# Kernel optimization log

Hardware: AMD Instinct MI355X
Metric: run time of the kernel (lower is better)

## Reference

```python
import jax, jax.numpy as jnp
import numpy as np

B, T = 64, 512
OBS, DM, DS, NL = 115, 128, 8, 3
EMB, NA, H1 = 16, 19, 256


def _ln(x, g, b, eps=1e-5):
    m = jnp.mean(x, -1, keepdims=True)
    v = jnp.mean((x - m) ** 2, -1, keepdims=True)
    return (x - m) * jax.lax.rsqrt(v + eps) * g + b


def _s6(x, h, lng, lnb, w_ig, w_dt, b_dt, a_log, w_b, w_c, d_par, w_out):
    # x: [B,T,DM], h: [B,DM,DS]
    xn = _ln(x, lng, lnb)
    xp = xn @ w_ig.T                               # [B,T,2*DM]
    x_in, z = xp[..., :DM], xp[..., DM:]
    dt = jax.nn.softplus(x_in @ w_dt.T + b_dt)     # [B,T,DM]
    A = -jnp.exp(a_log)                            # [DM,DS]
    bt = x_in @ w_b.T                              # [B,T,DS]
    ct = x_in @ w_c.T                              # [B,T,DS]
    dA = jnp.exp(dt[..., None] * A)                # [B,T,DM,DS]
    upd = (dt * x_in)[..., None] * bt[:, :, None, :]  # [B,T,DM,DS]

    def step(hc, inp):
        dA_t, u_t, c_t = inp
        hn = dA_t * hc + u_t                       # [B,DM,DS]
        y = jnp.einsum('bds,bs->bd', hn, c_t)      # [B,DM]
        return hn, y

    h_f, ys = jax.lax.scan(
        step, h,
        (jnp.swapaxes(dA, 0, 1), jnp.swapaxes(upd, 0, 1), jnp.swapaxes(ct, 0, 1)))
    y = jnp.swapaxes(ys, 0, 1)                     # [B,T,DM]
    ssm = y * jax.nn.silu(z) + x_in * d_par
    return x + ssm @ w_out.T, h_f.reshape(h_f.shape[0], -1)


def _forward(prev_actions, obs, h0, enc_w1, enc_b1, enc_g1, enc_bb1, enc_w2, enc_b2,
             enc_g2, enc_bb2, emb, proj_w, proj_b, proj_g, proj_bb,
             m_ln_g, m_ln_b, m_w_ig, m_w_dt, m_b_dt, m_a_log, m_w_b, m_w_c, m_d, m_w_out,
             fn_g, fn_b, pol_w1, pol_b1, pol_g, pol_bb, pol_w2, pol_b2):
    # MLP encoder: Linear -> LN -> SiLU -> Linear -> LN (final norm)
    e = jax.nn.silu(_ln(obs @ enc_w1.T + enc_b1, enc_g1, enc_bb1))
    e = _ln(e @ enc_w2.T + enc_b2, enc_g2, enc_bb2)
    pa = emb[prev_actions]                         # [B,T,EMB]
    x = jnp.concatenate([e, pa], -1) @ proj_w.T + proj_b
    x = jax.nn.silu(_ln(x, proj_g, proj_bb))
    for i in range(NL):
        x, _ = _s6(x, h0[i].reshape(-1, DM, DS), m_ln_g[i], m_ln_b[i], m_w_ig[i],
                   m_w_dt[i], m_b_dt[i], m_a_log[i], m_w_b[i], m_w_c[i], m_d[i], m_w_out[i])
    x = _ln(x, fn_g, fn_b)
    p = jax.nn.silu(_ln(x @ pol_w1.T + pol_b1, pol_g, pol_bb))
    return p @ pol_w2.T + pol_b2                   # [B,T,NA] policy logits


def setup_inputs() -> dict:
    key = jax.random.key(0)
    ks = iter(jax.random.split(key, 64))
    def n(shape, s=0.05):
        return jax.random.normal(next(ks), shape, dtype=jnp.float32) * s
    return {
        'obs': jax.random.normal(next(ks), (B, T, OBS), dtype=jnp.float32),
        'h0': jnp.zeros((NL, B, DM * DS), jnp.float32),
        'enc_w1': n((H1, OBS)), 'enc_b1': jnp.zeros((H1,)),
        'enc_g1': jnp.ones((H1,)), 'enc_bb1': jnp.zeros((H1,)),
        'enc_w2': n((DM, H1)), 'enc_b2': jnp.zeros((DM,)),
        'enc_g2': jnp.ones((DM,)), 'enc_bb2': jnp.zeros((DM,)),
        'emb': n((NA + 1, EMB), 1.0),
        'proj_w': n((DM, DM + EMB)), 'proj_b': jnp.zeros((DM,)),
        'proj_g': jnp.ones((DM,)), 'proj_bb': jnp.zeros((DM,)),
        'm_ln_g': jnp.ones((NL, DM)), 'm_ln_b': jnp.zeros((NL, DM)),
        'm_w_ig': n((NL, 2 * DM, DM)), 'm_w_dt': n((NL, DM, DM)),
        'm_b_dt': jnp.zeros((NL, DM)),
        'm_a_log': jax.random.uniform(next(ks), (NL, DM, DS), minval=-3.0, maxval=-1.0, dtype=jnp.float32),
        'm_w_b': n((NL, DS, DM)), 'm_w_c': n((NL, DS, DM)),
        'm_d': jnp.ones((NL, DM)), 'm_w_out': n((NL, DM, DM)),
        'fn_g': jnp.ones((DM,)), 'fn_b': jnp.zeros((DM,)),
        'pol_w1': n((DM, DM)), 'pol_b1': jnp.zeros((DM,)),
        'pol_g': jnp.ones((DM,)), 'pol_bb': jnp.zeros((DM,)),
        'pol_w2': n((NA, DM)), 'pol_b2': jnp.zeros((NA,)),
        'prev_actions': jax.random.randint(next(ks), (B, T), 0, NA + 1),
    }


def reference(obs, h0, enc_w1, enc_b1, enc_g1, enc_bb1, enc_w2, enc_b2, enc_g2, enc_bb2,
              emb, proj_w, proj_b, proj_g, proj_bb, m_ln_g, m_ln_b, m_w_ig, m_w_dt,
              m_b_dt, m_a_log, m_w_b, m_w_c, m_d, m_w_out, fn_g, fn_b, pol_w1, pol_b1,
              pol_g, pol_bb, pol_w2, pol_b2, prev_actions):
    return _forward(prev_actions, obs, h0, enc_w1, enc_b1, enc_g1, enc_bb1, enc_w2,
                    enc_b2, enc_g2, enc_bb2, emb, proj_w, proj_b, proj_g, proj_bb,
                    m_ln_g, m_ln_b, m_w_ig, m_w_dt, m_b_dt, m_a_log, m_w_b, m_w_c,
                    m_d, m_w_out, fn_g, fn_b, pol_w1, pol_b1, pol_g, pol_bb, pol_w2, pol_b2)
```

## Files before the change

kernel.cpp:

```cpp
#include <hip/hip_runtime.h>
#include <math.h>

#define BB 64
#define TT 512
#define OBSD 115
#define DMD 128
#define DSD 8
#define NLD 3
#define EMBD 16
#define NAD 19
#define H1D 256
#define NTOK (BB*TT)
#define SSEG 16
#define TSEG (TT/SSEG)

typedef unsigned short ushort_t;
typedef __attribute__((ext_vector_type(8))) short short8;
typedef __attribute__((ext_vector_type(4))) float f32x4;

__device__ __forceinline__ float silu_f(float x){ return x / (1.f + __expf(-x)); }
__device__ __forceinline__ float softplus_f(float x){
  return fmaxf(x, 0.f) + log1pf(__expf(-fabsf(x)));
}
__device__ __forceinline__ ushort_t f2bf(float x){
  unsigned u = __float_as_uint(x);
  unsigned r = (u + 0x7fffu + ((u >> 16) & 1u)) >> 16;
  return (ushort_t)r;
}
__device__ __forceinline__ float b2f(ushort_t x){
  return __uint_as_float(((unsigned)x) << 16);
}
#define MFMA(a,b,c) __builtin_amdgcn_mfma_f32_16x16x32_bf16((a),(b),(c),0,0,0)
#define LOG2E 1.44269504f

template<int D, int SV>
__device__ __forceinline__ void ln32(const float* s_val, float* s_mr, int tid){
  const int t = tid >> 3, part = tid & 7;
  float s = 0.f, s2 = 0.f;
  #pragma unroll
  for (int j = part; j < D; j += 8){ float v = s_val[t*SV + j]; s += v; s2 = fmaf(v, v, s2); }
  s += __shfl_xor(s, 1, 64); s2 += __shfl_xor(s2, 1, 64);
  s += __shfl_xor(s, 2, 64); s2 += __shfl_xor(s2, 2, 64);
  s += __shfl_xor(s, 4, 64); s2 += __shfl_xor(s2, 4, 64);
  if (part == 0){
    float m = s * (1.f/(float)D);
    s_mr[t*2] = m;
    s_mr[t*2+1] = rsqrtf(s2 * (1.f/(float)D) - m*m + 1e-5f);
  }
}

struct PJob { const float* src; ushort_t* dst; int N; int K; int Kpad; int rowofs; int Nw; };
struct PJobs { PJob j[20]; };

__global__ __launch_bounds__(256) void k_prep(PJobs P){
  const int job = blockIdx.x >> 2;
  const int sub = blockIdx.x & 3;
  PJob pj = P.j[job];
  const int elems = pj.Nw * pj.Kpad;
  for (int idx = sub*256 + threadIdx.x; idx < elems; idx += 4*256){
    int n = idx / pj.Kpad;
    int k = idx - n*pj.Kpad;
    float v = (n < pj.N && k < pj.K) ? pj.src[(size_t)n*pj.K + k] : 0.f;
    pj.dst[(size_t)(pj.rowofs + n)*pj.Kpad + k] = f2bf(v);
  }
}

__global__ __launch_bounds__(256) void k_enc1(
    const float* __restrict__ obs, const ushort_t* __restrict__ w1b,
    const float* __restrict__ b1, const float* __restrict__ g1,
    const float* __restrict__ bb1, ushort_t* __restrict__ e1)
{
  __shared__ __align__(16) char sm[34048];
  float*    s_val = (float*)sm;
  ushort_t* s_a   = (ushort_t*)sm;
  float*    s_mr  = (float*)(sm + 33792);
  const int tok0 = blockIdx.x * 32;
  const int tid = threadIdx.x;
  const int lane = tid & 63, w = tid >> 6;
  const int q = lane >> 4, cn = lane & 15;
  const int m0 = (w & 1) * 16, nh = w >> 1;

  for (int e = tid; e < 32*16; e += 256){
    int t = e >> 4, kc = e & 15;
    const float* op = obs + (size_t)(tok0 + t)*OBSD;
    short8 v;
    #pragma unroll
    for (int j = 0; j < 8; j++){
      int k = kc*8 + j;
      v[j] = (short)f2bf(k < OBSD ? op[k] : 0.f);
    }
    *(short8*)&s_a[t*136 + kc*8] = v;
  }
  __syncthreads();

  short8 af[4];
  #pragma unroll
  for (int ks = 0; ks < 4; ks++)
    af[ks] = *(const short8*)&s_a[(m0 + cn)*136 + ks*32 + q*8];
  __syncthreads();

  #pragma unroll
  for (int nt = 0; nt < 8; nt++){
    const int n0 = (nh*8 + nt) * 16;
    f32x4 acc = {0.f,0.f,0.f,0.f};
    #pragma unroll
    for (int ks = 0; ks < 4; ks++){
      short8 bf = *(const short8*)&w1b[(size_t)(n0 + cn)*128 + ks*32 + q*8];
      acc = MFMA(af[ks], bf, acc);
    }
    float bias = b1[n0 + cn];
    #pragma unroll
    for (int r = 0; r < 4; r++)
      s_val[(m0 + q*4 + r)*264 + n0 + cn] = acc[r] + bias;
  }
  __syncthreads();

  ln32<256,264>(s_val, s_mr, tid);
  __syncthreads();
  for (int e = tid; e < 32*256; e += 256){
    int t = e >> 8, c = e & 255;
    float v = (s_val[t*264 + c] - s_mr[t*2]) * s_mr[t*2+1] * g1[c] + bb1[c];
    e1[(size_t)(tok0 + t)*256 + c] = f2bf(silu_f(v));
  }
}

__global__ __launch_bounds__(256) void k_enc2p(
    const ushort_t* __restrict__ e1, const ushort_t* __restrict__ w2b,
    const float* __restrict__ b2, const float* __restrict__ g2,
    const float* __restrict__ bb2,
    const float* __restrict__ emb, const int* __restrict__ pact,
    const ushort_t* __restrict__ pwb, const float* __restrict__ pb,
    const float* __restrict__ pg, const float* __restrict__ pbb,
    float* __restrict__ X,
    const float* __restrict__ lng, const float* __restrict__ lnb,
    const ushort_t* __restrict__ wigb, const ushort_t* __restrict__ wdbcb,
    const float* __restrict__ bdt,
    ushort_t* __restrict__ XINb, ushort_t* __restrict__ Zb,
    ushort_t* __restrict__ DTb, ushort_t* __restrict__ BTu, ushort_t* __restrict__ CTu,
    const float* __restrict__ alog0,
    float* __restrict__ HLOC, float* __restrict__ PPR)
{
  __shared__ __align__(16) char sm[28928];
  float*    s_val = (float*)sm;
  ushort_t* s_xin = (ushort_t*)sm;
  ushort_t* s_dt  = (ushort_t*)(sm + 8704);
  ushort_t* s_a   = (ushort_t*)(sm + 17408);
  ushort_t* s_btc = (ushort_t*)(sm + 28160);
  float*    s_mr  = (float*)(sm + 28672);

  const int tok0 = blockIdx.x * 32;
  const int bidx = blockIdx.x >> 4;
  const int ch   = blockIdx.x & 15;
  const int tid = threadIdx.x;
  const int lane = tid & 63, w = tid >> 6;
  const int q = lane >> 4, cn = lane & 15;
  const int m0 = (w & 1) * 16, nh = w >> 1;

  for (int e = tid; e < 32*32; e += 256){
    int t = e >> 5, k = e & 31;
    float v = 0.f;
    if (k < EMBD){ int a = pact[tok0 + t]; v = emb[(size_t)a*EMBD + k]; }
    s_a[t*168 + 128 + k] = f2bf(v);
  }
  {
    short8 af[8];
    #pragma unroll
    for (int ks = 0; ks < 8; ks++)
      af[ks] = *(const short8*)&e1[(size_t)(tok0 + m0 + cn)*256 + ks*32 + q*8];
    #pragma unroll
    for (int nt = 0; nt < 4; nt++){
      const int n0 = (nh*4 + nt) * 16;
      f32x4 acc = {0.f,0.f,0.f,0.f};
      #pragma unroll
      for (int ks = 0; ks < 8; ks++){
        short8 bf = *(const short8*)&w2b[(size_t)(n0 + cn)*256 + ks*32 + q*8];
        acc = MFMA(af[ks], bf, acc);
      }
      float bias = b2[n0 + cn];
      #pragma unroll
      for (int r = 0; r < 4; r++)
        s_val[(m0 + q*4 + r)*136 + n0 + cn] = acc[r] + bias;
    }
  }
  __syncthreads();

  ln32<128,136>(s_val, s_mr, tid);
  __syncthreads();
  for (int e = tid; e < 32*128; e += 256){
    int t = e >> 7, c = e & 127;
    float v = (s_val[t*136 + c] - s_mr[t*2]) * s_mr[t*2+1] * g2[c] + bb2[c];
    s_a[t*168 + c] = f2bf(v);
  }
  __syncthreads();

  {
    short8 af2[5];
    #pragma unroll
    for (int ks = 0; ks < 5; ks++)
      af2[ks] = *(const short8*)&s_a[(m0 + cn)*168 + ks*32 + q*8];
    #pragma unroll
    for (int nt = 0; nt < 4; nt++){
      const int n0 = (nh*4 + nt) * 16;
      f32x4 acc = {0.f,0.f,0.f,0.f};
      #pragma unroll
      for (int ks = 0; ks < 5; ks++){
        short8 bf = *(const short8*)&pwb[(size_t)(n0 + cn)*160 + ks*32 + q*8];
        acc = MFMA(af2[ks], bf, acc);
      }
      float bias = pb[n0 + cn];
      #pragma unroll
      for (int r = 0; r < 4; r++)
        s_val[(m0 + q*4 + r)*136 + n0 + cn] = acc[r] + bias;
    }
  }
  __syncthreads();

  ln32<128,136>(s_val, s_mr, tid);
  __syncthreads();
  for (int e = tid; e < 32*128; e += 256){
    int t = e >> 7, c = e & 127;
    float v = (s_val[t*136 + c] - s_mr[t*2]) * s_mr[t*2+1] * pg[c] + pbb[c];
    v = silu_f(v);
    X[(size_t)tok0*128 + e] = v;
    s_val[t*136 + c] = v;
  }
  __syncthreads();

  ln32<128,136>(s_val, s_mr, tid);
  __syncthreads();
  for (int e = tid; e < 32*128; e += 256){
    int t = e >> 7, c = e & 127;
    float v = (s_val[t*136 + c] - s_mr[t*2]) * s_mr[t*2+1] * lng[c] + lnb[c];
    s_a[t*168 + c] = f2bf(v);
  }
  __syncthreads();

  {
    short8 af[4];
    #pragma unroll
    for (int ks = 0; ks < 4; ks++)
      af[ks] = *(const short8*)&s_a[(m0 + cn)*168 + ks*32 + q*8];
    #pragma unroll
    for (int nt = 0; nt < 8; nt++){
      const int n0 = (nh*8 + nt) * 16;
      f32x4 acc = {0.f,0.f,0.f,0.f};
      #pragma unroll
      for (int ks = 0; ks < 4; ks++){
        short8 bf = *(const short8*)&wigb[(size_t)(n0 + cn)*128 + ks*32 + q*8];
        acc = MFMA(af[ks], bf, acc);
      }
      if (n0 < 128){
        #pragma unroll
        for (int r = 0; r < 4; r++){
          int tr = m0 + q*4 + r;
          ushort_t bb = f2bf(acc[r]);
          XINb[(size_t)(tok0 + tr)*128 + n0 + cn] = bb;
          s_xin[tr*136 + n0 + cn] = bb;
        }
      } else {
        #pragma unroll
        for (int r = 0; r < 4; r++){
          int tr = m0 + q*4 + r;
          Zb[(size_t)(tok0 + tr)*128 + (n0 - 128) + cn] = f2bf(acc[r]);
        }
      }
    }
  }
  __syncthreads();

  {
    short8 af2[4];
    #pragma unroll
    for (int ks = 0; ks < 4; ks++)
      af2[ks] = *(const short8*)&s_xin[(m0 + cn)*136 + ks*32 + q*8];
    for (int nt = nh; nt < 9; nt += 2){
      const int n0 = nt * 16;
      f32x4 acc = {0.f,0.f,0.f,0.f};
      #pragma unroll
      for (int ks = 0; ks < 4; ks++){
        short8 bf = *(const short8*)&wdbcb[(size_t)(n0 + cn)*128 + ks*32 + q*8];
        acc = MFMA(af2[ks], bf, acc);
      }
      const int col = n0 + cn;
      if (col < 128){
        float bd = bdt[col];
        #pragma unroll
        for (int r = 0; r < 4; r++){
          int tr = m0 + q*4 + r;
          ushort_t dv = f2bf(softplus_f(acc[r] + bd));
          DTb[(size_t)(tok0 + tr)*128 + col] = dv;
          s_dt[tr*136 + col] = dv;
        }
      } else if (col < 136){
        #pragma unroll
        for (int r = 0; r < 4; r++){
          int tr = m0 + q*4 + r;
          ushort_t bb = f2bf(acc[r]);
          BTu[(size_t)(tok0 + tr)*8 + (col - 128)] = bb;
          s_btc[tr*8 + (col - 128)] = bb;
        }
      } else {
        #pragma unroll
        for (int r = 0; r < 4; r++)
          CTu[(size_t)(tok0 + m0 + q*4 + r)*8 + (col - 136)] = f2bf(acc[r]);
      }
    }
  }
  __syncthreads();

  {
    const int d = tid & 127, sh = tid >> 7;
    float A2c[4], hh[4], pp[4];
    #pragma unroll
    for (int j = 0; j < 4; j++){
      A2c[j] = -__expf(alog0[d*8 + sh*4 + j]) * LOG2E;
      hh[j] = 0.f; pp[j] = 1.f;
    }
    for (int t = 0; t < 32; t++){
      float dt = b2f(s_dt[t*136 + d]);
      float wv = dt * b2f(s_xin[t*136 + d]);
      #pragma unroll
      for (int j = 0; j < 4; j++){
        float dA = exp2f(dt * A2c[j]);
        hh[j] = fmaf(dA, hh[j], wv * b2f(s_btc[t*8 + sh*4 + j]));
        pp[j] *= dA;
      }
    }
    const size_t o = ((size_t)bidx*16 + ch)*1024 + d*8 + sh*4;
    #pragma unroll
    for (int j = 0; j < 4; j++){ HLOC[o+j] = hh[j]; PPR[o+j] = pp[j]; }
  }
}

#define SMS 26368

__device__ __forceinline__ void phaseB_post(
    const ushort_t* DTb, const ushort_t* XINb, const ushort_t* Zb,
    const ushort_t* BTu, const ushort_t* CTu,
    const float* __restrict__ alog, const float* __restrict__ h0g,
    const float* __restrict__ HLi, const float* __restrict__ PPi,
    const float* __restrict__ dpar, const ushort_t* __restrict__ woutb,
    float* __restrict__ X, char* sm, int b, int sg)
{
  ushort_t* s_dtS = (ushort_t*)sm;
  ushort_t* s_xiS = (ushort_t*)(sm + 8192);
  ushort_t* s_a   = (ushort_t*)(sm + 16384);
  float*    s_x   = (float*)sm;
  ushort_t* s_bt  = (ushort_t*)(sm + 25088);
  ushort_t* s_ct  = (ushort_t*)(sm + 25600);
  float*    s_mr  = (float*)(sm + 26112);

  const int tid = threadIdx.x;
  const int d = tid;
  const int w = tid >> 6, lane = tid & 63, q = lane >> 4, cn = lane & 15;
  const size_t segtok = (size_t)b*TT + sg*TSEG;

  {
    const uint4* gdt = (const uint4*)(DTb + segtok*128);
    const uint4* gxi = (const uint4*)(XINb + segtok*128);
    #pragma unroll
    for (int i = 0; i < 4; i++){
      ((uint4*)s_dtS)[tid + i*128] = gdt[tid + i*128];
      ((uint4*)s_xiS)[tid + i*128] = gxi[tid + i*128];
    }
    ((unsigned*)s_bt)[tid] = ((const unsigned*)(BTu + segtok*8))[tid];
    ((unsigned*)s_ct)[tid] = ((const unsigned*)(CTu + segtok*8))[tid];
  }
  float A2[8], h[8];
  #pragma unroll
  for (int s = 0; s < 8; s++){
    A2[s] = -__expf(alog[d*8 + s]) * LOG2E;
    h[s] = h0g[(size_t)b*1024 + d*8 + s];
  }
  for (int ch = 0; ch < sg; ch++){
    const size_t o = ((size_t)b*SSEG + ch)*1024 + d*8;
    float4 hl0 = *(const float4*)(HLi + o);
    float4 hl1 = *(const float4*)(HLi + o + 4);
    float4 pp0 = *(const float4*)(PPi + o);
    float4 pp1 = *(const float4*)(PPi + o + 4);
    h[0]=fmaf(pp0.x,h[0],hl0.x); h[1]=fmaf(pp0.y,h[1],hl0.y);
    h[2]=fmaf(pp0.z,h[2],hl0.z); h[3]=fmaf(pp0.w,h[3],hl0.w);
    h[4]=fmaf(pp1.x,h[4],hl1.x); h[5]=fmaf(pp1.y,h[5],hl1.y);
    h[6]=fmaf(pp1.z,h[6],hl1.z); h[7]=fmaf(pp1.w,h[7],hl1.w);
  }
  __syncthreads();

  #pragma unroll 4
  for (int t = 0; t < 32; t++){
    float dt = b2f(s_dtS[t*128 + d]);
    float xi = b2f(s_xiS[t*128 + d]);
    float wv = dt * xi;
    float y = 0.f;
    #pragma unroll
    for (int s = 0; s < 8; s++){
      float dA = exp2f(dt * A2[s]);
      h[s] = fmaf(dA, h[s], wv * b2f(s_bt[t*8 + s]));
      y = fmaf(h[s], b2f(s_ct[t*8 + s]), y);
    }
    s_a[t*136 + d] = f2bf(y);
  }
  __syncthreads();

  {
    const int c0 = (tid & 15)*8, trow = tid >> 4;
    float dpv[8];
    #pragma unroll
    for (int j = 0; j < 8; j++) dpv[j] = dpar[c0 + j];
    #pragma unroll
    for (int i = 0; i < 4; i++){
      const int t = trow + i*8;
      uint4 zb = ((const uint4*)(Zb + segtok*128))[tid + i*128];
      const ushort_t* zp = (const ushort_t*)&zb;
      #pragma unroll
      for (int j = 0; j < 8; j++){
        float y  = b2f(s_a[t*136 + c0 + j]);
        float xi = b2f(s_xiS[t*128 + c0 + j]);
        float ssm = y * silu_f(b2f(zp[j])) + xi * dpv[j];
        s_a[t*136 + c0 + j] = f2bf(ssm);
      }
    }
  }
  __syncthreads();

  {
    short8 af[2][4];
    #pragma unroll
    for (int mt = 0; mt < 2; mt++)
      #pragma unroll
      for (int ks = 0; ks < 4; ks++)
        af[mt][ks] = *(const short8*)&s_a[(mt*16 + cn)*136 + ks*32 + q*8];
    __syncthreads();
    for (int nt = w; nt < 8; nt += 2){
      const int n0 = nt * 16;
      short8 bf[4];
      #pragma unroll
      for (int ks = 0; ks < 4; ks++)
        bf[ks] = *(const short8*)&woutb[(size_t)(n0+cn)*128 + ks*32 + q*8];
      #pragma unroll
      for (int mt = 0; mt < 2; mt++){
        f32x4 acc = {0.f,0.f,0.f,0.f};
        #pragma unroll
        for (int ks = 0; ks < 4; ks++) acc = MFMA(af[mt][ks], bf[ks], acc);
        #pragma unroll
        for (int r = 0; r < 4; r++){
          const int tr = mt*16 + q*4 + r;
          const size_t g = (segtok + tr)*128 + n0 + cn;
          float xn = X[g] + acc[r];
          X[g] = xn;
          s_x[tr*130 + n0 + cn] = xn;
        }
      }
    }
  }
  __syncthreads();

  {
    const int t = tid >> 2, qtr = tid & 3;
    float s = 0.f, s2 = 0.f;
    const float* row = s_x + t*130 + qtr*32;
    for (int j = 0; j < 32; j++){ float v = row[j]; s += v; s2 = fmaf(v, v, s2); }
    s  += __shfl_xor(s, 1, 64);  s2 += __shfl_xor(s2, 1, 64);
    s  += __shfl_xor(s, 2, 64);  s2 += __shfl_xor(s2, 2, 64);
    float m = s * (1.f/128.f);
    float var = s2 * (1.f/128.f) - m*m;
    if (qtr == 0){ s_mr[t*2] = m; s_mr[t*2+1] = rsqrtf(var + 1e-5f); }
  }
  __syncthreads();
}

__global__ __launch_bounds__(128) void k_scan2p(
    ushort_t* DTb, ushort_t* XINb, ushort_t* Zb,
    ushort_t* BTu, ushort_t* CTu,
    const float* __restrict__ alog, const float* __restrict__ h0g,
    const float* __restrict__ HLi, const float* __restrict__ PPi,
    const float* __restrict__ dpar, const ushort_t* __restrict__ woutb,
    float* __restrict__ X,
    const float* __restrict__ lng, const float* __restrict__ lnb,
    const ushort_t* __restrict__ wigb, const ushort_t* __restrict__ wdbcb,
    const float* __restrict__ bdt,
    const float* __restrict__ alogn,
    float* __restrict__ HLo, float* __restrict__ PPo)
{
  __shared__ __align__(16) char sm[SMS];
  ushort_t* s_a  = (ushort_t*)(sm + 16384);
  float*    s_x  = (float*)sm;
  ushort_t* s_xin= (ushort_t*)sm;
  ushort_t* s_bt = (ushort_t*)(sm + 25088);
  float*    s_mr = (float*)(sm + 26112);

  const int b = blockIdx.x >> 4, sg = blockIdx.x & 15;
  const int tid = threadIdx.x;
  const int w = tid >> 6, lane = tid & 63, q = lane >> 4, cn = lane & 15;
  const size_t segtok = (size_t)b*TT + sg*TSEG;

  phaseB_post(DTb, XINb, Zb, BTu, CTu, alog, h0g, HLi, PPi, dpar, woutb, X, sm, b, sg);

  {
    float g = lng[tid], c0 = lnb[tid];
    float x31 = s_x[31*130 + tid];
    __syncthreads();
    for (int t = 0; t < 31; t++){
      float v = (s_x[t*130 + tid] - s_mr[t*2]) * s_mr[t*2+1] * g + c0;
      s_a[t*136 + tid] = f2bf(v);
    }
    float v = (x31 - s_mr[62]) * s_mr[63] * g + c0;
    s_a[31*136 + tid] = f2bf(v);
  }
  __syncthreads();

  {
    short8 af[2][4];
    #pragma unroll
    for (int mt = 0; mt < 2; mt++)
      #pragma unroll
      for (int ks = 0; ks < 4; ks++)
        af[mt][ks] = *(const short8*)&s_a[(mt*16 + cn)*136 + ks*32 + q*8];
    for (int nt = w; nt < 16; nt += 2){
      const int n0 = nt * 16;
      short8 bf[4];
      #pragma unroll
      for (int ks = 0; ks < 4; ks++)
        bf[ks] = *(const short8*)&wigb[(size_t)(n0+cn)*128 + ks*32 + q*8];
      #pragma unroll
      for (int mt = 0; mt < 2; mt++){
        f32x4 acc = {0.f,0.f,0.f,0.f};
        #pragma unroll
        for (int ks = 0; ks < 4; ks++) acc = MFMA(af[mt][ks], bf[ks], acc);
        if (n0 < 128){
          #pragma unroll
          for (int r = 0; r < 4; r++){
            const int tr = mt*16 + q*4 + r;
            ushort_t bb = f2bf(acc[r]);
            XINb[(segtok + tr)*128 + n0 + cn] = bb;
            s_xin[tr*136 + n0 + cn] = bb;
          }
        } else {
          #pragma unroll
          for (int r = 0; r < 4; r++){
            const int tr = mt*16 + q*4 + r;
            Zb[(segtok + tr)*128 + (n0-128) + cn] = f2bf(acc[r]);
          }
        }
      }
    }
  }
  __syncthreads();

  {
    short8 af[2][4];
    #pragma unroll
    for (int mt = 0; mt < 2; mt++)
      #pragma unroll
      for (int ks = 0; ks < 4; ks++)
        af[mt][ks] = *(const short8*)&s_xin[(mt*16 + cn)*136 + ks*32 + q*8];
    for (int nt = w; nt < 9; nt += 2){
      const int n0 = nt * 16;
      short8 bf[4];
      #pragma unroll
      for (int ks = 0; ks < 4; ks++)
        bf[ks] = *(const short8*)&wdbcb[(size_t)(n0+cn)*128 + ks*32 + q*8];
      const int col = n0 + cn;
      #pragma unroll
      for (int mt = 0; mt < 2; mt++){
        f32x4 acc = {0.f,0.f,0.f,0.f};
        #pragma unroll
        for (int ks = 0; ks < 4; ks++) acc = MFMA(af[mt][ks], bf[ks], acc);
        if (col < 128){
          float bd = bdt[col];
          #pragma unroll
          for (int r = 0; r < 4; r++){
            const int tr = mt*16 + q*4 + r;
            ushort_t dv = f2bf(softplus_f(acc[r] + bd));
            DTb[(segtok + tr)*128 + col] = dv;
            s_a[tr*136 + col] = dv;
          }
        } else if (col < 136){
          #pragma unroll
          for (int r = 0; r < 4; r++){
            const int tr = mt*16 + q*4 + r;
            ushort_t bb = f2bf(acc[r]);
            BTu[(segtok + tr)*8 + (col-128)] = bb;
            s_bt[tr*8 + (col-128)] = bb;
          }
        } else {
          #pragma unroll
          for (int r = 0; r < 4; r++)
            CTu[(segtok + mt*16 + q*4 + r)*8 + (col-136)] = f2bf(acc[r]);
        }
      }
    }
  }
  __syncthreads();

  {
    float A2n[8], hh[8], pp[8];
    #pragma unroll
    for (int s = 0; s < 8; s++){
      A2n[s] = -__expf(alogn[tid*8 + s]) * LOG2E;
      hh[s] = 0.f; pp[s] = 1.f;
    }
    for (int t = 0; t < 32; t++){
      float dt = b2f(s_a[t*136 + tid]);
      float wv = dt * b2f(s_xin[t*136 + tid]);
      #pragma unroll
      for (int s = 0; s < 8; s++){
        float dA = exp2f(dt * A2n[s]);
        hh[s] = fmaf(dA, hh[s], wv * b2f(s_bt[t*8 + s]));
        pp[s] *= dA;
      }
    }
    const size_t o = ((size_t)b*SSEG + sg)*1024 + tid*8;
    #pragma unroll
    for (int s = 0; s < 8; s++){ HLo[o+s] = hh[s]; PPo[o+s] = pp[s]; }
  }
}

__global__ __launch_bounds__(128) void k_scan2h(
    const ushort_t* DTb, const ushort_t* XINb, const ushort_t* Zb,
    const ushort_t* BTu, const ushort_t* CTu,
    const float* __restrict__ alog, const float* __restrict__ h0g,
    const float* __restrict__ HLi, const float* __restrict__ PPi,
    const float* __restrict__ dpar, const ushort_t* __restrict__ woutb,
    float* __restrict__ X,
    const float* __restrict__ fng, const float* __restrict__ fnb,
    const ushort_t* __restrict__ pw1b, const float* __restrict__ pb1,
    const float* __restrict__ pg, const float* __restrict__ pbb,
    const ushort_t* __restrict__ pw2b, const float* __restrict__ pb2,
    float* __restrict__ out)
{
  __shared__ __align__(16) char sm[SMS];
  ushort_t* s_a  = (ushort_t*)(sm + 16384);
  float*    s_x  = (float*)sm;
  float*    s_mr = (float*)(sm + 26112);

  const int b = blockIdx.x >> 4, sg = blockIdx.x & 15;
  const int tid = threadIdx.x;
  const int w = tid >> 6, lane = tid & 63, q = lane >> 4, cn = lane & 15;
  const size_t segtok = (size_t)b*TT + sg*TSEG;

  phaseB_post((ushort_t*)DTb, (ushort_t*)XINb, (ushort_t*)Zb,
              (ushort_t*)BTu, (ushort_t*)CTu, alog, h0g, HLi, PPi,
              dpar, woutb, X, sm, b, sg);

  {
    float g = fng[tid], c0 = fnb[tid];
    float x31 = s_x[31*130 + tid];
    __syncthreads();
    for (int t = 0; t < 31; t++){
      float v = (s_x[t*130 + tid] - s_mr[t*2]) * s_mr[t*2+1] * g + c0;
      s_a[t*136 + tid] = f2bf(v);
    }
    float v = (x31 - s_mr[62]) * s_mr[63] * g + c0;
    s_a[31*136 + tid] = f2bf(v);
  }
  __syncthreads();

  {
    short8 af[2][4];
    #pragma unroll
    for (int mt = 0; mt < 2; mt++)
      #pragma unroll
      for (int ks = 0; ks < 4; ks++)
        af[mt][ks] = *(const short8*)&s_a[(mt*16 + cn)*136 + ks*32 + q*8];
    __syncthreads();
    for (int nt = w; nt < 8; nt += 2){
      const int n0 = nt * 16;
      short8 bf[4];
      #pragma unroll
      for (int ks = 0; ks < 4; ks++)
        bf[ks] = *(const short8*)&pw1b[(size_t)(n0+cn)*128 + ks*32 + q*8];
      float bias = pb1[n0 + cn];
      #pragma unroll
      for (int mt = 0; mt < 2; mt++){
        f32x4 acc = {0.f,0.f,0.f,0.f};
        #pragma unroll
        for (int ks = 0; ks < 4; ks++) acc = MFMA(af[mt][ks], bf[ks], acc);
        #pragma unroll
        for (int r = 0; r < 4; r++)
          s_x[(mt*16 + q*4 + r)*130 + n0 + cn] = acc[r] + bias;
      }
    }
  }
  __syncthreads();

  {
    const int t = tid >> 2, qtr = tid & 3;
    float s = 0.f, s2 = 0.f;
    const float* row = s_x + t*130 + qtr*32;
    for (int j = 0; j < 32; j++){ float v = row[j]; s += v; s2 = fmaf(v, v, s2); }
    s  += __shfl_xor(s, 1, 64);  s2 += __shfl_xor(s2, 1, 64);
    s  += __shfl_xor(s, 2, 64);  s2 += __shfl_xor(s2, 2, 64);
    float m = s * (1.f/128.f);
    float var = s2 * (1.f/128.f) - m*m;
    if (qtr == 0){ s_mr[t*2] = m; s_mr[t*2+1] = rsqrtf(var + 1e-5f); }
  }
  __syncthreads();
  {
    float g = pg[tid], c0 = pbb[tid];
    float x31 = s_x[31*130 + tid];
    __syncthreads();
    for (int t = 0; t < 31; t++){
      float v = (s_x[t*130 + tid] - s_mr[t*2]) * s_mr[t*2+1] * g + c0;
      s_a[t*136 + tid] = f2bf(silu_f(v));
    }
    float v = (x31 - s_mr[62]) * s_mr[63] * g + c0;
    s_a[31*136 + tid] = f2bf(silu_f(v));
  }
  __syncthreads();

  {
    short8 af[2][4];
    #pragma unroll
    for (int mt = 0; mt < 2; mt++)
      #pragma unroll
      for (int ks = 0; ks < 4; ks++)
        af[mt][ks] = *(const short8*)&s_a[(mt*16 + cn)*136 + ks*32 + q*8];
    const int n0 = w * 16;
    short8 bf[4];
    #pragma unroll
    for (int ks = 0; ks < 4; ks++)
      bf[ks] = *(const short8*)&pw2b[(size_t)(n0+cn)*128 + ks*32 + q*8];
    const int col = n0 + cn;
    #pragma unroll
    for (int mt = 0; mt < 2; mt++){
      f32x4 acc = {0.f,0.f,0.f,0.f};
      #pragma unroll
      for (int ks = 0; ks < 4; ks++) acc = MFMA(af[mt][ks], bf[ks], acc);
      if (col < NAD){
        float bias = pb2[col];
        #pragma unroll
        for (int r = 0; r < 4; r++)
          out[(segtok + mt*16 + q*4 + r)*NAD + col] = acc[r] + bias;
      }
    }
  }
}

extern "C" void kernel_launch(void* const* d_in, const int* in_sizes, int n_in,
                              void* d_out, int out_size, void* d_ws, size_t ws_size,
                              hipStream_t stream) {
  const float* obs    = (const float*)d_in[0];
  const float* h0     = (const float*)d_in[1];
  const float* enc_w1 = (const float*)d_in[2];
  const float* enc_b1 = (const float*)d_in[3];
  const float* enc_g1 = (const float*)d_in[4];
  const float* enc_bb1= (const float*)d_in[5];
  const float* enc_w2 = (const float*)d_in[6];
  const float* enc_b2 = (const float*)d_in[7];
  const float* enc_g2 = (const float*)d_in[8];
  const float* enc_bb2= (const float*)d_in[9];
  const float* emb    = (const float*)d_in[10];
  const float* proj_w = (const float*)d_in[11];
  const float* proj_b = (const float*)d_in[12];
  const float* proj_g = (const float*)d_in[13];
  const float* proj_bb= (const float*)d_in[14];
  const float* m_ln_g = (const float*)d_in[15];
  const float* m_ln_b = (const float*)d_in[16];
  const float* m_w_ig = (const float*)d_in[17];
  const float* m_w_dt = (const float*)d_in[18];
  const float* m_b_dt = (const float*)d_in[19];
  const float* m_a_log= (const float*)d_in[20];
  const float* m_w_b  = (const float*)d_in[21];
  const float* m_w_c  = (const float*)d_in[22];
  const float* m_d    = (const float*)d_in[23];
  const float* m_w_out= (const float*)d_in[24];
  const float* fn_g   = (const float*)d_in[25];
  const float* fn_b   = (const float*)d_in[26];
  const float* pol_w1 = (const float*)d_in[27];
  const float* pol_b1 = (const float*)d_in[28];
  const float* pol_g  = (const float*)d_in[29];
  const float* pol_bb = (const float*)d_in[30];
  const float* pol_w2 = (const float*)d_in[31];
  const float* pol_b2 = (const float*)d_in[32];
  const int*   pact   = (const int*)d_in[33];

  float* ws  = (float*)d_ws;
  float* X    = ws;
  float* HLA  = X + (size_t)NTOK*128;
  float* PPA  = HLA + (size_t)BB*16*1024;
  float* HLB  = PPA + (size_t)BB*16*1024;
  float* PPB  = HLB + (size_t)BB*16*1024;
  ushort_t* E1   = (ushort_t*)(PPB + (size_t)BB*16*1024);
  ushort_t* XINb = E1   + (size_t)NTOK*256;
  ushort_t* Zb   = XINb + (size_t)NTOK*128;
  ushort_t* DTb  = Zb   + (size_t)NTOK*128;
  ushort_t* BTu  = DTb  + (size_t)NTOK*128;
  ushort_t* CTu  = BTu  + (size_t)NTOK*8;

  ushort_t* W1B   = CTu   + (size_t)NTOK*8;
  ushort_t* W2B   = W1B   + 256*128;
  ushort_t* PWB   = W2B   + 128*256;
  ushort_t* WIGB  = PWB   + 128*160;
  ushort_t* WDBCB = WIGB  + 3*256*128;
  ushort_t* WOUTB = WDBCB + 3*144*128;
  ushort_t* PW1B  = WOUTB + 3*128*128;
  ushort_t* PW2B  = PW1B  + 128*128;

  PJobs P;
  int nj = 0;
  auto add = [&](const float* src, ushort_t* dst, int N, int K, int Kpad, int rowofs, int Nw){
    P.j[nj].src = src; P.j[nj].dst = dst; P.j[nj].N = N; P.j[nj].K = K;
    P.j[nj].Kpad = Kpad; P.j[nj].rowofs = rowofs; P.j[nj].Nw = Nw; nj++;
  };
  add(enc_w1, W1B, 256, 115, 128, 0, 256);
  add(enc_w2, W2B, 128, 256, 256, 0, 128);
  add(proj_w, PWB, 128, 144, 160, 0, 128);
  for (int l = 0; l < NLD; l++)
    add(m_w_ig + (size_t)l*256*128, WIGB + (size_t)l*256*128, 256, 128, 128, 0, 256);
  for (int l = 0; l < NLD; l++){
    add(m_w_dt + (size_t)l*128*128, WDBCB + (size_t)l*144*128, 128, 128, 128, 0,   128);
    add(m_w_b  + (size_t)l*8*128,   WDBCB + (size_t)l*144*128,   8, 128, 128, 128,   8);
    add(m_w_c  + (size_t)l*8*128,   WDBCB + (size_t)l*144*128,   8, 128, 128, 136,   8);
  }
  for (int l = 0; l < NLD; l++)
    add(m_w_out + (size_t)l*128*128, WOUTB + (size_t)l*128*128, 128, 128, 128, 0, 128);
  add(pol_w1, PW1B, 128, 128, 128, 0, 128);
  add(pol_w2, PW2B,  19, 128, 128, 0,  32);

  k_prep<<<20*4, 256, 0, stream>>>(P);
  k_enc1<<<NTOK/32, 256, 0, stream>>>(obs, W1B, enc_b1, enc_g1, enc_bb1, E1);
  k_enc2p<<<NTOK/32, 256, 0, stream>>>(E1, W2B, enc_b2, enc_g2, enc_bb2,
      emb, pact, PWB, proj_b, proj_g, proj_bb, X,
      m_ln_g, m_ln_b, WIGB, WDBCB, m_b_dt,
      XINb, Zb, DTb, BTu, CTu,
      m_a_log, HLA, PPA);

  k_scan2p<<<BB*SSEG, 128, 0, stream>>>(DTb, XINb, Zb, BTu, CTu,
      m_a_log, h0, HLA, PPA, m_d, WOUTB, X,
      m_ln_g + 128, m_ln_b + 128,
      WIGB + (size_t)256*128, WDBCB + (size_t)144*128, m_b_dt + 128,
      m_a_log + 1024, HLB, PPB);
  k_scan2p<<<BB*SSEG, 128, 0, stream>>>(DTb, XINb, Zb, BTu, CTu,
      m_a_log + 1024, h0 + (size_t)BB*1024, HLB, PPB, m_d + 128,
      WOUTB + (size_t)128*128, X,
      m_ln_g + 256, m_ln_b + 256,
      WIGB + (size_t)2*256*128, WDBCB + (size_t)2*144*128, m_b_dt + 256,
      m_a_log + 2048, HLA, PPA);
  k_scan2h<<<BB*SSEG, 128, 0, stream>>>(DTb, XINb, Zb, BTu, CTu,
      m_a_log + 2048, h0 + (size_t)2*BB*1024, HLA, PPA, m_d + 256,
      WOUTB + (size_t)2*128*128, X,
      fn_g, fn_b, PW1B, pol_b1, pol_g, pol_bb, PW2B, pol_b2,
      (float*)d_out);
}
```

Baseline: 401.2 us.

## Split scan into 32 segments of 16 tokens per block

```diff
diff --git a/kernel.cpp b/kernel.cpp
--- a/kernel.cpp
+++ b/kernel.cpp
@@ -11,7 +11,7 @@
 #define NAD 19
 #define H1D 256
 #define NTOK (BB*TT)
-#define SSEG 16
+#define SSEG 32
 #define TSEG (TT/SSEG)
 
 typedef unsigned short ushort_t;
@@ -310,29 +310,31 @@
 
   {
     const int d = tid & 127, sh = tid >> 7;
-    float A2c[4], hh[4], pp[4];
-    #pragma unroll
-    for (int j = 0; j < 4; j++){
+    float A2c[4];
+    #pragma unroll
+    for (int j = 0; j < 4; j++)
       A2c[j] = -__expf(alog0[d*8 + sh*4 + j]) * LOG2E;
-      hh[j] = 0.f; pp[j] = 1.f;
-    }
-    for (int t = 0; t < 32; t++){
-      float dt = b2f(s_dt[t*136 + d]);
-      float wv = dt * b2f(s_xin[t*136 + d]);
-      #pragma unroll
-      for (int j = 0; j < 4; j++){
-        float dA = exp2f(dt * A2c[j]);
-        hh[j] = fmaf(dA, hh[j], wv * b2f(s_btc[t*8 + sh*4 + j]));
-        pp[j] *= dA;
-      }
-    }
-    const size_t o = ((size_t)bidx*16 + ch)*1024 + d*8 + sh*4;
-    #pragma unroll
-    for (int j = 0; j < 4; j++){ HLOC[o+j] = hh[j]; PPR[o+j] = pp[j]; }
-  }
-}
-
-#define SMS 26368
+    #pragma unroll
+    for (int half = 0; half < 2; half++){
+      float hh[4] = {0.f,0.f,0.f,0.f}, pp[4] = {1.f,1.f,1.f,1.f};
+      for (int t = half*16; t < half*16 + 16; t++){
+        float dt = b2f(s_dt[t*136 + d]);
+        float wv = dt * b2f(s_xin[t*136 + d]);
+        #pragma unroll
+        for (int j = 0; j < 4; j++){
+          float dA = exp2f(dt * A2c[j]);
+          hh[j] = fmaf(dA, hh[j], wv * b2f(s_btc[t*8 + sh*4 + j]));
+          pp[j] *= dA;
+        }
+      }
+      const size_t o = ((size_t)bidx*SSEG + ch*2 + half)*1024 + d*8 + sh*4;
+      #pragma unroll
+      for (int j = 0; j < 4; j++){ HLOC[o+j] = hh[j]; PPR[o+j] = pp[j]; }
+    }
+  }
+}
+
+#define SMS 13184
 
 __device__ __forceinline__ void phaseB_post(
     const ushort_t* DTb, const ushort_t* XINb, const ushort_t* Zb,
@@ -343,12 +345,12 @@
     float* __restrict__ X, char* sm, int b, int sg)
 {
   ushort_t* s_dtS = (ushort_t*)sm;
-  ushort_t* s_xiS = (ushort_t*)(sm + 8192);
-  ushort_t* s_a   = (ushort_t*)(sm + 16384);
+  ushort_t* s_xiS = (ushort_t*)(sm + 4096);
+  ushort_t* s_a   = (ushort_t*)(sm + 8192);
   float*    s_x   = (float*)sm;
-  ushort_t* s_bt  = (ushort_t*)(sm + 25088);
-  ushort_t* s_ct  = (ushort_t*)(sm + 25600);
-  float*    s_mr  = (float*)(sm + 26112);
+  ushort_t* s_bt  = (ushort_t*)(sm + 12544);
+  ushort_t* s_ct  = (ushort_t*)(sm + 12800);
+  float*    s_mr  = (float*)(sm + 13056);
 
   const int tid = threadIdx.x;
   const int d = tid;
@@ -359,12 +361,14 @@
     const uint4* gdt = (const uint4*)(DTb + segtok*128);
     const uint4* gxi = (const uint4*)(XINb + segtok*128);
     #pragma unroll
-    for (int i = 0; i < 4; i++){
+    for (int i = 0; i < 2; i++){
       ((uint4*)s_dtS)[tid + i*128] = gdt[tid + i*128];
       ((uint4*)s_xiS)[tid + i*128] = gxi[tid + i*128];
     }
-    ((unsigned*)s_bt)[tid] = ((const unsigned*)(BTu + segtok*8))[tid];
-    ((unsigned*)s_ct)[tid] = ((const unsigned*)(CTu + segtok*8))[tid];
+    if (tid < 64){
+      ((unsigned*)s_bt)[tid] = ((const unsigned*)(BTu + segtok*8))[tid];
+      ((unsigned*)s_ct)[tid] = ((const unsigned*)(CTu + segtok*8))[tid];
+    }
   }
   float A2[8], h[8];
   #pragma unroll
@@ -386,7 +390,7 @@
   __syncthreads();
 
   #pragma unroll 4
-  for (int t = 0; t < 32; t++){
+  for (int t = 0; t < TSEG; t++){
     float dt = b2f(s_dtS[t*128 + d]);
     float xi = b2f(s_xiS[t*128 + d]);
     float wv = dt * xi;
@@ -407,7 +411,7 @@
     #pragma unroll
     for (int j = 0; j < 8; j++) dpv[j] = dpar[c0 + j];
     #pragma unroll
-    for (int i = 0; i < 4; i++){
+    for (int i = 0; i < 2; i++){
       const int t = trow + i*8;
       uint4 zb = ((const uint4*)(Zb + segtok*128))[tid + i*128];
       const ushort_t* zp = (const ushort_t*)&zb;
@@ -423,12 +427,10 @@
   __syncthreads();
 
   {
-    short8 af[2][4];
-    #pragma unroll
-    for (int mt = 0; mt < 2; mt++)
-      #pragma unroll
-      for (int ks = 0; ks < 4; ks++)
-        af[mt][ks] = *(const short8*)&s_a[(mt*16 + cn)*136 + ks*32 + q*8];
+    short8 af[4];
+    #pragma unroll
+    for (int ks = 0; ks < 4; ks++)
+      af[ks] = *(const short8*)&s_a[cn*136 + ks*32 + q*8];
     __syncthreads();
     for (int nt = w; nt < 8; nt += 2){
       const int n0 = nt * 16;
@@ -436,36 +438,53 @@
       #pragma unroll
       for (int ks = 0; ks < 4; ks++)
         bf[ks] = *(const short8*)&woutb[(size_t)(n0+cn)*128 + ks*32 + q*8];
-      #pragma unroll
-      for (int mt = 0; mt < 2; mt++){
-        f32x4 acc = {0.f,0.f,0.f,0.f};
-        #pragma unroll
-        for (int ks = 0; ks < 4; ks++) acc = MFMA(af[mt][ks], bf[ks], acc);
-        #pragma unroll
-        for (int r = 0; r < 4; r++){
-          const int tr = mt*16 + q*4 + r;
-          const size_t g = (segtok + tr)*128 + n0 + cn;
-          float xn = X[g] + acc[r];
-          X[g] = xn;
-          s_x[tr*130 + n0 + cn] = xn;
-        }
-      }
-    }
-  }
-  __syncthreads();
-
-  {
-    const int t = tid >> 2, qtr = tid & 3;
+      f32x4 acc = {0.f,0.f,0.f,0.f};
+      #pragma unroll
+      for (int ks = 0; ks < 4; ks++) acc = MFMA(af[ks], bf[ks], acc);
+      #pragma unroll
+      for (int r = 0; r < 4; r++){
+        const int tr = q*4 + r;
+        const size_t g = (segtok + tr)*128 + n0 + cn;
+        float xn = X[g] + acc[r];
+        X[g] = xn;
+        s_x[tr*130 + n0 + cn] = xn;
+      }
+    }
+  }
+  __syncthreads();
+
+  {
+    const int t = tid >> 3, part = tid & 7;
     float s = 0.f, s2 = 0.f;
-    const float* row = s_x + t*130 + qtr*32;
-    for (int j = 0; j < 32; j++){ float v = row[j]; s += v; s2 = fmaf(v, v, s2); }
-    s  += __shfl_xor(s, 1, 64);  s2 += __shfl_xor(s2, 1, 64);
-    s  += __shfl_xor(s, 2, 64);  s2 += __shfl_xor(s2, 2, 64);
-    float m = s * (1.f/128.f);
-    float var = s2 * (1.f/128.f) - m*m;
-    if (qtr == 0){ s_mr[t*2] = m; s_mr[t*2+1] = rsqrtf(var + 1e-5f); }
-  }
-  __syncthreads();
+    #pragma unroll
+    for (int j = part; j < 128; j += 8){ float v = s_x[t*130 + j]; s += v; s2 = fmaf(v, v, s2); }
+    s += __shfl_xor(s, 1, 64); s2 += __shfl_xor(s2, 1, 64);
+    s += __shfl_xor(s, 2, 64); s2 += __shfl_xor(s2, 2, 64);
+    s += __shfl_xor(s, 4, 64); s2 += __shfl_xor(s2, 4, 64);
+    if (part == 0){
+      float m = s * (1.f/128.f);
+      s_mr[t*2] = m;
+      s_mr[t*2+1] = rsqrtf(s2*(1.f/128.f) - m*m + 1e-5f);
+    }
+  }
+  __syncthreads();
+}
+
+__device__ __forceinline__ void norm16(const float* s_x, const float* s_mr,
+    ushort_t* s_a, const float* __restrict__ gv, const float* __restrict__ bv,
+    int tid, bool dosilu)
+{
+  float g = gv[tid], c0 = bv[tid];
+  float x15 = s_x[15*130 + tid];
+  __syncthreads();
+  for (int t = 0; t < 15; t++){
+    float v = (s_x[t*130 + tid] - s_mr[t*2]) * s_mr[t*2+1] * g + c0;
+    if (dosilu) v = silu_f(v);
+    s_a[t*136 + tid] = f2bf(v);
+  }
+  float v = (x15 - s_mr[30]) * s_mr[31] * g + c0;
+  if (dosilu) v = silu_f(v);
+  s_a[15*136 + tid] = f2bf(v);
 }
 
 __global__ __launch_bounds__(128) void k_scan2p(
@@ -482,77 +501,60 @@
     float* __restrict__ HLo, float* __restrict__ PPo)
 {
   __shared__ __align__(16) char sm[SMS];
-  ushort_t* s_a  = (ushort_t*)(sm + 16384);
+  ushort_t* s_a  = (ushort_t*)(sm + 8192);
   float*    s_x  = (float*)sm;
   ushort_t* s_xin= (ushort_t*)sm;
-  ushort_t* s_bt = (ushort_t*)(sm + 25088);
-  float*    s_mr = (float*)(sm + 26112);
-
-  const int b = blockIdx.x >> 4, sg = blockIdx.x & 15;
+  ushort_t* s_bt = (ushort_t*)(sm + 12544);
+  float*    s_mr = (float*)(sm + 13056);
+
+  const int b = blockIdx.x >> 5, sg = blockIdx.x & 31;
   const int tid = threadIdx.x;
   const int w = tid >> 6, lane = tid & 63, q = lane >> 4, cn = lane & 15;
   const size_t segtok = (size_t)b*TT + sg*TSEG;
 
   phaseB_post(DTb, XINb, Zb, BTu, CTu, alog, h0g, HLi, PPi, dpar, woutb, X, sm, b, sg);
 
-  {
-    float g = lng[tid], c0 = lnb[tid];
-    float x31 = s_x[31*130 + tid];
-    __syncthreads();
-    for (int t = 0; t < 31; t++){
-      float v = (s_x[t*130 + tid] - s_mr[t*2]) * s_mr[t*2+1] * g + c0;
-      s_a[t*136 + tid] = f2bf(v);
-    }
-    float v = (x31 - s_mr[62]) * s_mr[63] * g + c0;
-    s_a[31*136 + tid] = f2bf(v);
-  }
-  __syncthreads();
-
-  {
-    short8 af[2][4];
-    #pragma unroll
-    for (int mt = 0; mt < 2; mt++)
-      #pragma unroll
-      for (int ks = 0; ks < 4; ks++)
-        af[mt][ks] = *(const short8*)&s_a[(mt*16 + cn)*136 + ks*32 + q*8];
+  norm16(s_x, s_mr, s_a, lng, lnb, tid, false);
+  __syncthreads();
+
+  {
+    short8 af[4];
+    #pragma unroll
+    for (int ks = 0; ks < 4; ks++)
+      af[ks] = *(const short8*)&s_a[cn*136 + ks*32 + q*8];
     for (int nt = w; nt < 16; nt += 2){
       const int n0 = nt * 16;
       short8 bf[4];
       #pragma unroll
       for (int ks = 0; ks < 4; ks++)
         bf[ks] = *(const short8*)&wigb[(size_t)(n0+cn)*128 + ks*32 + q*8];
-      #pragma unroll
-      for (int mt = 0; mt < 2; mt++){
-        f32x4 acc = {0.f,0.f,0.f,0.f};
-        #pragma unroll
-        for (int ks = 0; ks < 4; ks++) acc = MFMA(af[mt][ks], bf[ks], acc);
-        if (n0 < 128){
-          #pragma unroll
-          for (int r = 0; r < 4; r++){
-            const int tr = mt*16 + q*4 + r;
-            ushort_t bb = f2bf(acc[r]);
-            XINb[(segtok + tr)*128 + n0 + cn] = bb;
-            s_xin[tr*136 + n0 + cn] = bb;
-          }
-        } else {
-          #pragma unroll
-          for (int r = 0; r < 4; r++){
-            const int tr = mt*16 + q*4 + r;
-            Zb[(segtok + tr)*128 + (n0-128) + cn] = f2bf(acc[r]);
-          }
+      f32x4 acc = {0.f,0.f,0.f,0.f};
+      #pragma unroll
+      for (int ks = 0; ks < 4; ks++) acc = MFMA(af[ks], bf[ks], acc);
+      if (n0 < 128){
+        #pragma unroll
+        for (int r = 0; r < 4; r++){
+          const int tr = q*4 + r;
+          ushort_t bb = f2bf(acc[r]);
+          XINb[(segtok + tr)*128 + n0 + cn] = bb;
+          s_xin[tr*136 + n0 + cn] = bb;
         }
-      }
-    }
-  }
-  __syncthreads();
-
-  {
-    short8 af[2][4];
-    #pragma unroll
-    for (int mt = 0; mt < 2; mt++)
-      #pragma unroll
-      for (int ks = 0; ks < 4; ks++)
-        af[mt][ks] = *(const short8*)&s_xin[(mt*16 + cn)*136 + ks*32 + q*8];
+      } else {
+        #pragma unroll
+        for (int r = 0; r < 4; r++){
+          const int tr = q*4 + r;
+          Zb[(segtok + tr)*128 + (n0-128) + cn] = f2bf(acc[r]);
+        }
+      }
+    }
+  }
+  __syncthreads();
+
+  {
+    short8 af[4];
+    #pragma unroll
+    for (int ks = 0; ks < 4; ks++)
+      af[ks] = *(const short8*)&s_xin[cn*136 + ks*32 + q*8];
     for (int nt = w; nt < 9; nt += 2){
       const int n0 = nt * 16;
       short8 bf[4];
@@ -560,33 +562,30 @@
       for (int ks = 0; ks < 4; ks++)
         bf[ks] = *(const short8*)&wdbcb[(size_t)(n0+cn)*128 + ks*32 + q*8];
       const int col = n0 + cn;
-      #pragma unroll
-      for (int mt = 0; mt < 2; mt++){
-        f32x4 acc = {0.f,0.f,0.f,0.f};
-        #pragma unroll
-        for (int ks = 0; ks < 4; ks++) acc = MFMA(af[mt][ks], bf[ks], acc);
-        if (col < 128){
-          float bd = bdt[col];
-          #pragma unroll
-          for (int r = 0; r < 4; r++){
-            const int tr = mt*16 + q*4 + r;
-            ushort_t dv = f2bf(softplus_f(acc[r] + bd));
-            DTb[(segtok + tr)*128 + col] = dv;
-            s_a[tr*136 + col] = dv;
-          }
-        } else if (col < 136){
-          #pragma unroll
-          for (int r = 0; r < 4; r++){
-            const int tr = mt*16 + q*4 + r;
-            ushort_t bb = f2bf(acc[r]);
-            BTu[(segtok + tr)*8 + (col-128)] = bb;
-            s_bt[tr*8 + (col-128)] = bb;
-          }
-        } else {
-          #pragma unroll
-          for (int r = 0; r < 4; r++)
-            CTu[(segtok + mt*16 + q*4 + r)*8 + (col-136)] = f2bf(acc[r]);
+      f32x4 acc = {0.f,0.f,0.f,0.f};
+      #pragma unroll
+      for (int ks = 0; ks < 4; ks++) acc = MFMA(af[ks], bf[ks], acc);
+      if (col < 128){
+        float bd = bdt[col];
+        #pragma unroll
+        for (int r = 0; r < 4; r++){
+          const int tr = q*4 + r;
+          ushort_t dv = f2bf(softplus_f(acc[r] + bd));
+          DTb[(segtok + tr)*128 + col] = dv;
+          s_a[tr*136 + col] = dv;
         }
+      } else if (col < 136){
+        #pragma unroll
+        for (int r = 0; r < 4; r++){
+          const int tr = q*4 + r;
+          ushort_t bb = f2bf(acc[r]);
+          BTu[(segtok + tr)*8 + (col-128)] = bb;
+          s_bt[tr*8 + (col-128)] = bb;
+        }
+      } else {
+        #pragma unroll
+        for (int r = 0; r < 4; r++)
+          CTu[(segtok + q*4 + r)*8 + (col-136)] = f2bf(acc[r]);
       }
     }
   }
@@ -599,7 +598,7 @@
       A2n[s] = -__expf(alogn[tid*8 + s]) * LOG2E;
       hh[s] = 0.f; pp[s] = 1.f;
     }
-    for (int t = 0; t < 32; t++){
+    for (int t = 0; t < TSEG; t++){
       float dt = b2f(s_a[t*136 + tid]);
       float wv = dt * b2f(s_xin[t*136 + tid]);
       #pragma unroll
@@ -629,11 +628,11 @@
     float* __restrict__ out)
 {
   __shared__ __align__(16) char sm[SMS];
-  ushort_t* s_a  = (ushort_t*)(sm + 16384);
+  ushort_t* s_a  = (ushort_t*)(sm + 8192);
   float*    s_x  = (float*)sm;
-  float*    s_mr = (float*)(sm + 26112);
-
-  const int b = blockIdx.x >> 4, sg = blockIdx.x & 15;
+  float*    s_mr = (float*)(sm + 13056);
+
+  const int b = blockIdx.x >> 5, sg = blockIdx.x & 31;
   const int tid = threadIdx.x;
   const int w = tid >> 6, lane = tid & 63, q = lane >> 4, cn = lane & 15;
   const size_t segtok = (size_t)b*TT + sg*TSEG;
@@ -642,26 +641,14 @@
               (ushort_t*)BTu, (ushort_t*)CTu, alog, h0g, HLi, PPi,
               dpar, woutb, X, sm, b, sg);
 
-  {
-    float g = fng[tid], c0 = fnb[tid];
-    float x31 = s_x[31*130 + tid];
-    __syncthreads();
-    for (int t = 0; t < 31; t++){
-      float v = (s_x[t*130 + tid] - s_mr[t*2]) * s_mr[t*2+1] * g + c0;
-      s_a[t*136 + tid] = f2bf(v);
-    }
-    float v = (x31 - s_mr[62]) * s_mr[63] * g + c0;
-    s_a[31*136 + tid] = f2bf(v);
-  }
-  __syncthreads();
-
-  {
-    short8 af[2][4];
-    #pragma unroll
-    for (int mt = 0; mt < 2; mt++)
-      #pragma unroll
-      for (int ks = 0; ks < 4; ks++)
-        af[mt][ks] = *(const short8*)&s_a[(mt*16 + cn)*136 + ks*32 + q*8];
+  norm16(s_x, s_mr, s_a, fng, fnb, tid, false);
+  __syncthreads();
+
+  {
+    short8 af[4];
+    #pragma unroll
+    for (int ks = 0; ks < 4; ks++)
+      af[ks] = *(const short8*)&s_a[cn*136 + ks*32 + q*8];
     __syncthreads();
     for (int nt = w; nt < 8; nt += 2){
       const int n0 = nt * 16;
@@ -670,68 +657,53 @@
       for (int ks = 0; ks < 4; ks++)
         bf[ks] = *(const short8*)&pw1b[(size_t)(n0+cn)*128 + ks*32 + q*8];
       float bias = pb1[n0 + cn];
-      #pragma unroll
-      for (int mt = 0; mt < 2; mt++){
-        f32x4 acc = {0.f,0.f,0.f,0.f};
-        #pragma unroll
-        for (int ks = 0; ks < 4; ks++) acc = MFMA(af[mt][ks], bf[ks], acc);
-        #pragma unroll
-        for (int r = 0; r < 4; r++)
-          s_x[(mt*16 + q*4 + r)*130 + n0 + cn] = acc[r] + bias;
-      }
-    }
-  }
-  __syncthreads();
-
-  {
-    const int t = tid >> 2, qtr = tid & 3;
+      f32x4 acc = {0.f,0.f,0.f,0.f};
+      #pragma unroll
+      for (int ks = 0; ks < 4; ks++) acc = MFMA(af[ks], bf[ks], acc);
+      #pragma unroll
+      for (int r = 0; r < 4; r++)
+        s_x[(q*4 + r)*130 + n0 + cn] = acc[r] + bias;
+    }
+  }
+  __syncthreads();
+
+  {
+    const int t = tid >> 3, part = tid & 7;
     float s = 0.f, s2 = 0.f;
-    const float* row = s_x + t*130 + qtr*32;
-    for (int j = 0; j < 32; j++){ float v = row[j]; s += v; s2 = fmaf(v, v, s2); }
-    s  += __shfl_xor(s, 1, 64);  s2 += __shfl_xor(s2, 1, 64);
-    s  += __shfl_xor(s, 2, 64);  s2 += __shfl_xor(s2, 2, 64);
-    float m = s * (1.f/128.f);
-    float var = s2 * (1.f/128.f) - m*m;
-    if (qtr == 0){ s_mr[t*2] = m; s_mr[t*2+1] = rsqrtf(var + 1e-5f); }
-  }
-  __syncthreads();
-  {
-    float g = pg[tid], c0 = pbb[tid];
-    float x31 = s_x[31*130 + tid];
-    __syncthreads();
-    for (int t = 0; t < 31; t++){
-      float v = (s_x[t*130 + tid] - s_mr[t*2]) * s_mr[t*2+1] * g + c0;
-      s_a[t*136 + tid] = f2bf(silu_f(v));
-    }
-    float v = (x31 - s_mr[62]) * s_mr[63] * g + c0;
-    s_a[31*136 + tid] = f2bf(silu_f(v));
-  }
-  __syncthreads();
-
-  {
-    short8 af[2][4];
-    #pragma unroll
-    for (int mt = 0; mt < 2; mt++)
-      #pragma unroll
-      for (int ks = 0; ks < 4; ks++)
-        af[mt][ks] = *(const short8*)&s_a[(mt*16 + cn)*136 + ks*32 + q*8];
+    #pragma unroll
+    for (int j = part; j < 128; j += 8){ float v = s_x[t*130 + j]; s += v; s2 = fmaf(v, v, s2); }
+    s += __shfl_xor(s, 1, 64); s2 += __shfl_xor(s2, 1, 64);
+    s += __shfl_xor(s, 2, 64); s2 += __shfl_xor(s2, 2, 64);
+    s += __shfl_xor(s, 4, 64); s2 += __shfl_xor(s2, 4, 64);
+    if (part == 0){
+      float m = s * (1.f/128.f);
+      s_mr[t*2] = m;
+      s_mr[t*2+1] = rsqrtf(s2*(1.f/128.f) - m*m + 1e-5f);
+    }
+  }
+  __syncthreads();
+  norm16(s_x, s_mr, s_a, pg, pbb, tid, true);
+  __syncthreads();
+
+  {
+    short8 af[4];
+    #pragma unroll
+    for (int ks = 0; ks < 4; ks++)
+      af[ks] = *(const short8*)&s_a[cn*136 + ks*32 + q*8];
     const int n0 = w * 16;
     short8 bf[4];
     #pragma unroll
     for (int ks = 0; ks < 4; ks++)
       bf[ks] = *(const short8*)&pw2b[(size_t)(n0+cn)*128 + ks*32 + q*8];
     const int col = n0 + cn;
-    #pragma unroll
-    for (int mt = 0; mt < 2; mt++){
-      f32x4 acc = {0.f,0.f,0.f,0.f};
-      #pragma unroll
-      for (int ks = 0; ks < 4; ks++) acc = MFMA(af[mt][ks], bf[ks], acc);
-      if (col < NAD){
-        float bias = pb2[col];
-        #pragma unroll
-        for (int r = 0; r < 4; r++)
-          out[(segtok + mt*16 + q*4 + r)*NAD + col] = acc[r] + bias;
-      }
+    f32x4 acc = {0.f,0.f,0.f,0.f};
+    #pragma unroll
+    for (int ks = 0; ks < 4; ks++) acc = MFMA(af[ks], bf[ks], acc);
+    if (col < NAD){
+      float bias = pb2[col];
+      #pragma unroll
+      for (int r = 0; r < 4; r++)
+        out[(segtok + q*4 + r)*NAD + col] = acc[r] + bias;
     }
   }
 }
@@ -777,10 +749,10 @@
   float* ws  = (float*)d_ws;
   float* X    = ws;
   float* HLA  = X + (size_t)NTOK*128;
-  float* PPA  = HLA + (size_t)BB*16*1024;
-  float* HLB  = PPA + (size_t)BB*16*1024;
-  float* PPB  = HLB + (size_t)BB*16*1024;
-  ushort_t* E1   = (ushort_t*)(PPB + (size_t)BB*16*1024);
+  float* PPA  = HLA + (size_t)BB*SSEG*1024;
+  float* HLB  = PPA + (size_t)BB*SSEG*1024;
+  float* PPB  = HLB + (size_t)BB*SSEG*1024;
+  ushort_t* E1   = (ushort_t*)(PPB + (size_t)BB*SSEG*1024);
   ushort_t* XINb = E1   + (size_t)NTOK*256;
   ushort_t* Zb   = XINb + (size_t)NTOK*128;
   ushort_t* DTb  = Zb   + (size_t)NTOK*128;
```

After: 466.9 us. 16.4% more time.
